# Kernel optimization log

Measured on AMD Instinct MI355X. Metric: run time of the kernel, lower is better.

## Reference

```python
import jax, jax.numpy as jnp
import numpy as np

SEQ, B, CIN, H, K = 2048, 16, 512, 512, 2

def setup_inputs() -> dict:
    key = jax.random.key(0)
    k1, k2, k3 = jax.random.split(key, 3)
    x = jax.random.normal(k1, (SEQ, B, CIN), dtype=jnp.float32)
    W = jax.random.normal(k2, (3 * H, CIN, K), dtype=jnp.float32) * (1.0 / np.sqrt(CIN * K))
    b = jax.random.normal(k3, (3 * H,), dtype=jnp.float32) * 0.01
    return {"x": x, "W": W, "b": b}

def _qrnn_fo(x, W, b):
    # x: (T, B, Cin) -> conv input (B, Cin, T), causal left pad of K-1 zeros
    xb = jnp.transpose(x, (1, 2, 0))
    g = jax.lax.conv_general_dilated(
        xb, W, window_strides=(1,), padding=[(K - 1, 0)],
        dimension_numbers=("NCH", "OIH", "NCH"))
    g = g + b[None, :, None]
    g = jnp.transpose(g, (2, 0, 1))  # (T, B, 3H)
    zg, fg, og = jnp.split(g, 3, axis=-1)
    z = jnp.tanh(zg)
    f = jax.nn.sigmoid(fg)
    o = jax.nn.sigmoid(og)

    def step(c, gates_t):
        zt, ft, ot = gates_t
        c = ft * c + (1.0 - ft) * zt
        h = c * ot
        return c, h

    c0 = jnp.zeros((B, H), dtype=x.dtype)
    c_last, hs = jax.lax.scan(step, c0, (z, f, o))
    return hs, c_last

def reference(x, W, b):
    hs, c_last = _qrnn_fo(x, W, b)
    h_last = hs[-1]
    return hs, h_last[None, :], c_last[None, :]
```

## Files before the change

### kernel.cpp

```cpp
#include <hip/hip_runtime.h>

#define SEQ   2048
#define BATCH 16
#define CINCH 512
#define HDIM  512
#define NDIM  1536
#define TBM   (SEQ*BATCH)
#define KRED  1024
#define NCH   32
#define CHL   64
#define NCOL  8192

typedef unsigned short ushort_t;
typedef __bf16 bf16x8 __attribute__((ext_vector_type(8)));
typedef unsigned short u16x8 __attribute__((ext_vector_type(8)));
typedef float f32x4 __attribute__((ext_vector_type(4)));

__device__ __forceinline__ float bf2f(ushort_t u) {
    return __uint_as_float(((unsigned int)u) << 16);
}
__device__ __forceinline__ ushort_t f2bf(float x) {
    unsigned int u = __float_as_uint(x);
    unsigned int r = u + 0x7fffu + ((u >> 16) & 1u);
    return (ushort_t)(r >> 16);
}

__global__ void cast_x_kernel(const float* __restrict__ x, ushort_t* __restrict__ xb) {
    int i = blockIdx.x * 256 + threadIdx.x;
    int e = i * 4;
    ushort4 r;
    if (e < BATCH * CINCH) {
        r.x = 0; r.y = 0; r.z = 0; r.w = 0;
    } else {
        float4 v = *(const float4*)(x + (e - BATCH * CINCH));
        r.x = f2bf(v.x); r.y = f2bf(v.y); r.z = f2bf(v.z); r.w = f2bf(v.w);
    }
    *(ushort4*)(xb + e) = r;
}

__global__ void repack_w_kernel(const float* __restrict__ W, ushort_t* __restrict__ wb) {
    int i = blockIdx.x * 256 + threadIdx.x;
    int o  = i >> 10;
    int r  = i & 1023;
    int k  = r >> 9;
    int ci = r & 511;
    wb[i] = f2bf(W[o * 1024 + ci * 2 + k]);
}

__device__ __forceinline__ void load_lds_16B(const ushort_t* g, ushort_t* l) {
    auto* gp = reinterpret_cast<const __attribute__((address_space(1))) unsigned int*>(
        reinterpret_cast<uintptr_t>(g));
    auto* lp = reinterpret_cast<__attribute__((address_space(3))) unsigned int*>(
        reinterpret_cast<uintptr_t>(l));
    __builtin_amdgcn_global_load_lds(gp, lp, 16, 0, 0);
}

__global__ __launch_bounds__(256) void gemm_gates_kernel(
    const ushort_t* __restrict__ xb, const ushort_t* __restrict__ wb,
    const float* __restrict__ bias,
    ushort_t* __restrict__ zb, ushort_t* __restrict__ fb, ushort_t* __restrict__ ob) {

    __shared__ ushort_t smem[2 * 128 * 64];
    ushort_t* As = smem;
    ushort_t* Bs = smem + 128 * 64;

    const int tid  = threadIdx.x;
    const int w    = tid >> 6;
    const int lane = tid & 63;
    const int quad = lane >> 4;
    const int l15  = lane & 15;
    const int wm   = w & 1;
    const int wn   = w >> 1;
    const int mBase = blockIdx.x * 128;
    const int nBase = blockIdx.y * 128;

    const int srow = lane >> 3;
    const int scb  = lane & 7;

    f32x4 acc[4][4];
#pragma unroll
    for (int i = 0; i < 4; ++i)
#pragma unroll
        for (int j = 0; j < 4; ++j)
            acc[i][j] = (f32x4){0.f, 0.f, 0.f, 0.f};

    for (int kt = 0; kt < 16; ++kt) {
        __syncthreads();
        const long aOff = (kt < 8) ? (long)kt * 64 : (long)16 * 512 + (long)(kt - 8) * 64;
#pragma unroll
        for (int i = 0; i < 4; ++i) {
            const int row = w * 32 + i * 8 + srow;
            const int cbd = scb ^ (row & 7);
            const ushort_t* ga = xb + (long)(mBase + row) * 512 + aOff + cbd * 8;
            load_lds_16B(ga, &As[(w * 32 + i * 8) * 64]);
            const ushort_t* gb = wb + (long)(nBase + row) * 1024 + kt * 64 + cbd * 8;
            load_lds_16B(gb, &Bs[(w * 32 + i * 8) * 64]);
        }
        __syncthreads();

#pragma unroll
        for (int ks = 0; ks < 2; ++ks) {
            bf16x8 af[4], bfr[4];
            const int cbd = ks * 4 + quad;
#pragma unroll
            for (int mt = 0; mt < 4; ++mt) {
                int ml  = wm * 64 + mt * 16 + l15;
                int off = ml * 64 + ((cbd ^ (ml & 7)) * 8);
                af[mt] = __builtin_bit_cast(bf16x8, *(const u16x8*)(&As[off]));
            }
#pragma unroll
            for (int nt = 0; nt < 4; ++nt) {
                int nl  = wn * 64 + nt * 16 + l15;
                int off = nl * 64 + ((cbd ^ (nl & 7)) * 8);
                bfr[nt] = __builtin_bit_cast(bf16x8, *(const u16x8*)(&Bs[off]));
            }
#pragma unroll
            for (int mt = 0; mt < 4; ++mt)
#pragma unroll
                for (int nt = 0; nt < 4; ++nt)
                    acc[mt][nt] = __builtin_amdgcn_mfma_f32_16x16x32_bf16(
                        af[mt], bfr[nt], acc[mt][nt], 0, 0, 0);
        }
    }

    const int gate = nBase >> 9;
    const int hb   = nBase & 511;

    __syncthreads();
#pragma unroll
    for (int nt = 0; nt < 4; ++nt) {
        const int n_local = wn * 64 + nt * 16 + l15;
        const float bv = bias[nBase + n_local];
#pragma unroll
        for (int mt = 0; mt < 4; ++mt) {
#pragma unroll
            for (int r = 0; r < 4; ++r) {
                const int m_local = wm * 64 + mt * 16 + quad * 4 + r;
                float g = acc[mt][nt][r] + bv;
                float a;
                if (gate == 0) {
                    float e = __expf(-2.f * fabsf(g));
                    float t = (1.f - e) / (1.f + e);
                    a = copysignf(t, g);
                } else {
                    a = 1.f / (1.f + __expf(-g));
                }
                const int phys = ((n_local >> 3) ^ (m_local & 7)) * 8 + (n_local & 7);
                smem[m_local * 128 + phys] = f2bf(a);
            }
        }
    }
    __syncthreads();

    ushort_t* outp = (gate == 0) ? zb : (gate == 1) ? fb : ob;
#pragma unroll
    for (int s = 0; s < 8; ++s) {
        const int m_local = w * 32 + s * 4 + quad;
        const int blk = l15 ^ (m_local & 7);
        u16x8 v = *(const u16x8*)(&smem[m_local * 128 + blk * 8]);
        *(u16x8*)(outp + (long)(mBase + m_local) * 512 + hb + l15 * 8) = v;
    }
}

__global__ __launch_bounds__(256) void scan_compose(
    const ushort_t* __restrict__ zb, const ushort_t* __restrict__ fb,
    float* __restrict__ Acomp, float* __restrict__ Bcomp) {
    const int col = (blockIdx.x & 31) * 256 + threadIdx.x;
    const int ch  = blockIdx.x >> 5;
    const long base = (long)ch * CHL * NCOL + col;
    float A = 1.f, Bv = 0.f;
    const int U = 16;
    for (int w0 = 0; w0 < CHL; w0 += U) {
        float zc[U], fc[U];
#pragma unroll
        for (int u = 0; u < U; ++u) {
            long idx = base + (long)(w0 + u) * NCOL;
            zc[u] = bf2f(zb[idx]); fc[u] = bf2f(fb[idx]);
        }
#pragma unroll
        for (int u = 0; u < U; ++u) {
            Bv = fc[u] * Bv + (1.f - fc[u]) * zc[u];
            A *= fc[u];
        }
    }
    Acomp[ch * NCOL + col] = A;
    Bcomp[ch * NCOL + col] = Bv;
}

__global__ void scan_prefix(const float* __restrict__ Acomp,
                            const float* __restrict__ Bcomp,
                            float* __restrict__ Cin) {
    const int col = blockIdx.x * 256 + threadIdx.x;
    float c = 0.f;
#pragma unroll 4
    for (int ch = 0; ch < NCH; ++ch) {
        Cin[ch * NCOL + col] = c;
        c = Acomp[ch * NCOL + col] * c + Bcomp[ch * NCOL + col];
    }
}

__global__ __launch_bounds__(256) void scan_apply(
    const ushort_t* __restrict__ zb, const ushort_t* __restrict__ fb,
    const ushort_t* __restrict__ ob, const float* __restrict__ Cin,
    float* __restrict__ out) {
    const int col = (blockIdx.x & 31) * 256 + threadIdx.x;
    const int ch  = blockIdx.x >> 5;
    const long base = (long)ch * CHL * NCOL + col;
    float c = Cin[ch * NCOL + col];
    float h = 0.f;
    const int U = 16;
    for (int w0 = 0; w0 < CHL; w0 += U) {
        float zc[U], fc[U], oc[U];
#pragma unroll
        for (int u = 0; u < U; ++u) {
            long idx = base + (long)(w0 + u) * NCOL;
            zc[u] = bf2f(zb[idx]); fc[u] = bf2f(fb[idx]); oc[u] = bf2f(ob[idx]);
        }
#pragma unroll
        for (int u = 0; u < U; ++u) {
            c = fc[u] * c + (1.f - fc[u]) * zc[u];
            h = c * oc[u];
            out[base + (long)(w0 + u) * NCOL] = h;
        }
    }
    if (ch == NCH - 1) {
        out[(long)SEQ * NCOL + col] = h;
        out[(long)SEQ * NCOL + NCOL + col] = c;
    }
}

extern "C" void kernel_launch(void* const* d_in, const int* in_sizes, int n_in,
                              void* d_out, int out_size, void* d_ws, size_t ws_size,
                              hipStream_t stream) {
    const float* x  = (const float*)d_in[0];
    const float* W  = (const float*)d_in[1];
    const float* bi = (const float*)d_in[2];
    float* out = (float*)d_out;

    char* ws = (char*)d_ws;
    const size_t xbN = (size_t)(TBM + BATCH) * CINCH;
    const size_t wbN = (size_t)NDIM * KRED;
    const size_t gN  = (size_t)TBM * HDIM;
    ushort_t* xb = (ushort_t*)ws;
    ushort_t* wb = (ushort_t*)(ws + xbN * 2);
    ushort_t* zb = (ushort_t*)(ws + xbN * 2 + wbN * 2);
    ushort_t* fb = zb + gN;
    ushort_t* ob = fb + gN;
    float* Acomp = (float*)ws;
    float* Bcomp = Acomp + NCH * NCOL;
    float* Cin   = Bcomp + NCH * NCOL;

    cast_x_kernel<<<16392, 256, 0, stream>>>(x, xb);
    repack_w_kernel<<<6144, 256, 0, stream>>>(W, wb);
    dim3 ggrid(TBM / 128, NDIM / 128);
    gemm_gates_kernel<<<ggrid, 256, 0, stream>>>(xb, wb, bi, zb, fb, ob);
    scan_compose<<<NCH * 32, 256, 0, stream>>>(zb, fb, Acomp, Bcomp);
    scan_prefix<<<NCOL / 256, 256, 0, stream>>>(Acomp, Bcomp, Cin);
    scan_apply<<<NCH * 32, 256, 0, stream>>>(zb, fb, ob, Cin, out);
}
```

Before: 292.6 us.

## Fuse prep kernels, swap GEMM grid order, vectorize chunked scan with shorter chunks

Merges the x cast and weight repack into one launch, with the cast now handling 8 elements per thread. Swaps the GEMM grid axes so consecutive blocks walk the N dimension and share the same A rows in cache. Rewrites the scan kernels so each thread processes 8 adjacent columns using 16-byte vector loads and stores, with a one-step prefetch. The chunks become shorter and more numerous (128 chunks of 16 steps), which raises parallelism but lengthens the serial prefix pass and the compose/prefix buffers. Those larger buffers alias the xb workspace, which is fine because xb is dead by the time the scan runs.

Result: slower. 309.9 us (+5.9%).

```diff
diff --git a/kernel.cpp b/kernel.cpp
--- a/kernel.cpp
+++ b/kernel.cpp
@@ -7,8 +7,8 @@
 #define NDIM  1536
 #define TBM   (SEQ*BATCH)
 #define KRED  1024
-#define NCH   32
-#define CHL   64
+#define NCH   128
+#define CHL   16
 #define NCOL  8192
 
 typedef unsigned short ushort_t;
@@ -25,26 +25,31 @@
     return (ushort_t)(r >> 16);
 }
 
-__global__ void cast_x_kernel(const float* __restrict__ x, ushort_t* __restrict__ xb) {
-    int i = blockIdx.x * 256 + threadIdx.x;
-    int e = i * 4;
-    ushort4 r;
-    if (e < BATCH * CINCH) {
-        r.x = 0; r.y = 0; r.z = 0; r.w = 0;
+#define CAST_BLK 8196
+#define RPK_BLK  6144
+__global__ void prep_kernel(const float* __restrict__ x, ushort_t* __restrict__ xb,
+                            const float* __restrict__ W, ushort_t* __restrict__ wb) {
+    if (blockIdx.x < CAST_BLK) {
+        int e = (blockIdx.x * 256 + threadIdx.x) * 8;
+        u16x8 r;
+        if (e < BATCH * CINCH) {
+            r = (u16x8){0, 0, 0, 0, 0, 0, 0, 0};
+        } else {
+            const float* p = x + (e - BATCH * CINCH);
+            float4 v0 = *(const float4*)p;
+            float4 v1 = *(const float4*)(p + 4);
+            r[0] = f2bf(v0.x); r[1] = f2bf(v0.y); r[2] = f2bf(v0.z); r[3] = f2bf(v0.w);
+            r[4] = f2bf(v1.x); r[5] = f2bf(v1.y); r[6] = f2bf(v1.z); r[7] = f2bf(v1.w);
+        }
+        *(u16x8*)(xb + e) = r;
     } else {
-        float4 v = *(const float4*)(x + (e - BATCH * CINCH));
-        r.x = f2bf(v.x); r.y = f2bf(v.y); r.z = f2bf(v.z); r.w = f2bf(v.w);
-    }
-    *(ushort4*)(xb + e) = r;
-}
-
-__global__ void repack_w_kernel(const float* __restrict__ W, ushort_t* __restrict__ wb) {
-    int i = blockIdx.x * 256 + threadIdx.x;
-    int o  = i >> 10;
-    int r  = i & 1023;
-    int k  = r >> 9;
-    int ci = r & 511;
-    wb[i] = f2bf(W[o * 1024 + ci * 2 + k]);
+        int i = (blockIdx.x - CAST_BLK) * 256 + threadIdx.x;
+        int o  = i >> 10;
+        int r  = i & 1023;
+        int k  = r >> 9;
+        int ci = r & 511;
+        wb[i] = f2bf(W[o * 1024 + ci * 2 + k]);
+    }
 }
 
 __device__ __forceinline__ void load_lds_16B(const ushort_t* g, ushort_t* l) {
@@ -71,8 +76,8 @@
     const int l15  = lane & 15;
     const int wm   = w & 1;
     const int wn   = w >> 1;
-    const int mBase = blockIdx.x * 128;
-    const int nBase = blockIdx.y * 128;
+    const int nBase = blockIdx.x * 128;
+    const int mBase = blockIdx.y * 128;
 
     const int srow = lane >> 3;
     const int scb  = lane & 7;
@@ -165,26 +170,39 @@
 __global__ __launch_bounds__(256) void scan_compose(
     const ushort_t* __restrict__ zb, const ushort_t* __restrict__ fb,
     float* __restrict__ Acomp, float* __restrict__ Bcomp) {
-    const int col = (blockIdx.x & 31) * 256 + threadIdx.x;
-    const int ch  = blockIdx.x >> 5;
-    const long base = (long)ch * CHL * NCOL + col;
-    float A = 1.f, Bv = 0.f;
-    const int U = 16;
-    for (int w0 = 0; w0 < CHL; w0 += U) {
-        float zc[U], fc[U];
-#pragma unroll
-        for (int u = 0; u < U; ++u) {
-            long idx = base + (long)(w0 + u) * NCOL;
-            zc[u] = bf2f(zb[idx]); fc[u] = bf2f(fb[idx]);
-        }
-#pragma unroll
-        for (int u = 0; u < U; ++u) {
-            Bv = fc[u] * Bv + (1.f - fc[u]) * zc[u];
-            A *= fc[u];
-        }
-    }
-    Acomp[ch * NCOL + col] = A;
-    Bcomp[ch * NCOL + col] = Bv;
+    const int ch   = blockIdx.x >> 2;
+    const int col0 = (((blockIdx.x & 3) * 256) + threadIdx.x) * 8;
+    const long base = (long)ch * CHL * NCOL + col0;
+
+    float A[8], Bv[8];
+#pragma unroll
+    for (int j = 0; j < 8; ++j) { A[j] = 1.f; Bv[j] = 0.f; }
+
+    u16x8 zc = *(const u16x8*)(zb + base);
+    u16x8 fc = *(const u16x8*)(fb + base);
+    for (int t = 0; t < CHL; ++t) {
+        u16x8 zn, fn;
+        if (t + 1 < CHL) {
+            zn = *(const u16x8*)(zb + base + (long)(t + 1) * NCOL);
+            fn = *(const u16x8*)(fb + base + (long)(t + 1) * NCOL);
+        }
+#pragma unroll
+        for (int j = 0; j < 8; ++j) {
+            float f = bf2f(fc[j]), z = bf2f(zc[j]);
+            Bv[j] = f * Bv[j] + (1.f - f) * z;
+            A[j] *= f;
+        }
+        zc = zn; fc = fn;
+    }
+#pragma unroll
+    for (int j = 0; j < 4; ++j) {
+    }
+    f32x4 a0 = {A[0], A[1], A[2], A[3]}, a1 = {A[4], A[5], A[6], A[7]};
+    f32x4 b0 = {Bv[0], Bv[1], Bv[2], Bv[3]}, b1 = {Bv[4], Bv[5], Bv[6], Bv[7]};
+    *(f32x4*)(Acomp + (long)ch * NCOL + col0)     = a0;
+    *(f32x4*)(Acomp + (long)ch * NCOL + col0 + 4) = a1;
+    *(f32x4*)(Bcomp + (long)ch * NCOL + col0)     = b0;
+    *(f32x4*)(Bcomp + (long)ch * NCOL + col0 + 4) = b1;
 }
 
 __global__ void scan_prefix(const float* __restrict__ Acomp,
@@ -203,29 +221,44 @@
     const ushort_t* __restrict__ zb, const ushort_t* __restrict__ fb,
     const ushort_t* __restrict__ ob, const float* __restrict__ Cin,
     float* __restrict__ out) {
-    const int col = (blockIdx.x & 31) * 256 + threadIdx.x;
-    const int ch  = blockIdx.x >> 5;
-    const long base = (long)ch * CHL * NCOL + col;
-    float c = Cin[ch * NCOL + col];
-    float h = 0.f;
-    const int U = 16;
-    for (int w0 = 0; w0 < CHL; w0 += U) {
-        float zc[U], fc[U], oc[U];
-#pragma unroll
-        for (int u = 0; u < U; ++u) {
-            long idx = base + (long)(w0 + u) * NCOL;
-            zc[u] = bf2f(zb[idx]); fc[u] = bf2f(fb[idx]); oc[u] = bf2f(ob[idx]);
-        }
-#pragma unroll
-        for (int u = 0; u < U; ++u) {
-            c = fc[u] * c + (1.f - fc[u]) * zc[u];
-            h = c * oc[u];
-            out[base + (long)(w0 + u) * NCOL] = h;
-        }
+    const int ch   = blockIdx.x >> 2;
+    const int col0 = (((blockIdx.x & 3) * 256) + threadIdx.x) * 8;
+    const long base = (long)ch * CHL * NCOL + col0;
+
+    float c[8], h[8];
+    f32x4 c0 = *(const f32x4*)(Cin + (long)ch * NCOL + col0);
+    f32x4 c1 = *(const f32x4*)(Cin + (long)ch * NCOL + col0 + 4);
+    c[0] = c0[0]; c[1] = c0[1]; c[2] = c0[2]; c[3] = c0[3];
+    c[4] = c1[0]; c[5] = c1[1]; c[6] = c1[2]; c[7] = c1[3];
+
+    u16x8 zc = *(const u16x8*)(zb + base);
+    u16x8 fc = *(const u16x8*)(fb + base);
+    u16x8 oc = *(const u16x8*)(ob + base);
+    for (int t = 0; t < CHL; ++t) {
+        u16x8 zn, fn, on;
+        if (t + 1 < CHL) {
+            zn = *(const u16x8*)(zb + base + (long)(t + 1) * NCOL);
+            fn = *(const u16x8*)(fb + base + (long)(t + 1) * NCOL);
+            on = *(const u16x8*)(ob + base + (long)(t + 1) * NCOL);
+        }
+#pragma unroll
+        for (int j = 0; j < 8; ++j) {
+            float f = bf2f(fc[j]), z = bf2f(zc[j]), o = bf2f(oc[j]);
+            c[j] = f * c[j] + (1.f - f) * z;
+            h[j] = c[j] * o;
+        }
+        f32x4 h0 = {h[0], h[1], h[2], h[3]}, h1 = {h[4], h[5], h[6], h[7]};
+        *(f32x4*)(out + base + (long)t * NCOL)     = h0;
+        *(f32x4*)(out + base + (long)t * NCOL + 4) = h1;
+        zc = zn; fc = fn; oc = on;
     }
     if (ch == NCH - 1) {
-        out[(long)SEQ * NCOL + col] = h;
-        out[(long)SEQ * NCOL + NCOL + col] = c;
+        f32x4 h0 = {h[0], h[1], h[2], h[3]}, h1 = {h[4], h[5], h[6], h[7]};
+        f32x4 cc0 = {c[0], c[1], c[2], c[3]}, cc1 = {c[4], c[5], c[6], c[7]};
+        *(f32x4*)(out + (long)SEQ * NCOL + col0)            = h0;
+        *(f32x4*)(out + (long)SEQ * NCOL + col0 + 4)        = h1;
+        *(f32x4*)(out + (long)SEQ * NCOL + NCOL + col0)     = cc0;
+        *(f32x4*)(out + (long)SEQ * NCOL + NCOL + col0 + 4) = cc1;
     }
 }
 
@@ -250,11 +283,10 @@
     float* Bcomp = Acomp + NCH * NCOL;
     float* Cin   = Bcomp + NCH * NCOL;
 
-    cast_x_kernel<<<16392, 256, 0, stream>>>(x, xb);
-    repack_w_kernel<<<6144, 256, 0, stream>>>(W, wb);
-    dim3 ggrid(TBM / 128, NDIM / 128);
+    prep_kernel<<<CAST_BLK + RPK_BLK, 256, 0, stream>>>(x, xb, W, wb);
+    dim3 ggrid(NDIM / 128, TBM / 128);
     gemm_gates_kernel<<<ggrid, 256, 0, stream>>>(xb, wb, bi, zb, fb, ob);
-    scan_compose<<<NCH * 32, 256, 0, stream>>>(zb, fb, Acomp, Bcomp);
+    scan_compose<<<NCH * 4, 256, 0, stream>>>(zb, fb, Acomp, Bcomp);
     scan_prefix<<<NCOL / 256, 256, 0, stream>>>(Acomp, Bcomp, Cin);
-    scan_apply<<<NCH * 32, 256, 0, stream>>>(zb, fb, ob, Cin, out);
-}
+    scan_apply<<<NCH * 4, 256, 0, stream>>>(zb, fb, ob, Cin, out);
+}
```
